# Kernel tuning notes

Hardware: AMD Instinct MI355X
Metric: run time of the kernel (lower is better)

Reference implementation:

```python
import jax, jax.numpy as jnp
import numpy as np
from jax import lax

B, L, N, D, H = 32, 128, 64, 64, 4
DH = D // H


def lstm_seq(x, Wih, Whh, b, h0, c0):
    # x: [T, B, I]; PyTorch gate order i, f, g, o; bias b = b_ih + b_hh fused.
    def step(carry, xt):
        h, c = carry
        g = xt @ Wih.T + h @ Whh.T + b  # [B, 4D]
        i, f, gg, o = jnp.split(g, 4, axis=-1)
        c = jax.nn.sigmoid(f) * c + jax.nn.sigmoid(i) * jnp.tanh(gg)
        h = jax.nn.sigmoid(o) * jnp.tanh(c)
        return (h, c), h
    _, Hs = lax.scan(step, (h0, c0), x)
    return Hs  # [T, B, D]


def encode_one(x, Wih, Whh, b, pw, pb):
    # x: [T, B, 1] single variable series; per-variable LSTM encoder + temporal attn pool
    z0 = jnp.zeros((x.shape[1], Whh.shape[1]), x.dtype)
    Hs = lstm_seq(x, Wih, Whh, b, z0, z0)        # [T, B, D]
    a = jax.nn.softmax(Hs @ pw + pb, axis=0)      # softmax over time -> [T, B]
    return jnp.einsum('tb,tbd->bd', a, Hs)        # [B, D]


def decode_one(cs, Wih, Whh, b, Wh, bh, Wc, bc, ow, ob):
    # cs: [B, D]; all-zero input sequence of length L
    h0 = jnp.tanh(cs @ Wh.T + bh)
    c0 = jnp.tanh(cs @ Wc.T + bc)
    z = jnp.zeros((L, cs.shape[0], 1), cs.dtype)
    Ys = lstm_seq(z, Wih, Whh, b, h0, c0)         # [L, B, D]
    return Ys @ ow + ob                           # [L, B]


def forward(X, enc_Wih, enc_Whh, enc_b, pool_w, pool_b,
            attn_Wqkv, attn_bqkv, attn_Wo, attn_bo,
            dec_Wih, dec_Whh, dec_b, init_h_W, init_h_b, init_c_W, init_c_b,
            out_w, out_b):
    # ---- per-variable encoders (vmapped over N distinct weight sets) ----
    Xe = jnp.transpose(X[:, :L - 1, :], (2, 1, 0))[..., None]  # [N, L-1, B, 1]
    C = jax.vmap(encode_one)(Xe, enc_Wih, enc_Whh, enc_b, pool_w, pool_b)  # [N, B, D]
    C = jnp.transpose(C, (1, 0, 2))  # [B, N, D]

    # ---- cross-variable MHSA (nn.MultiheadAttention, dropout=0) ----
    qkv = C @ attn_Wqkv.T + attn_bqkv            # [B, N, 3D]
    q, k, v = jnp.split(qkv, 3, axis=-1)
    def heads(t):
        return jnp.transpose(t.reshape(B, N, H, DH), (0, 2, 1, 3))  # [B, H, N, DH]
    q, k, v = heads(q), heads(k), heads(v)
    attn = jax.nn.softmax(jnp.einsum('bhnd,bhmd->bhnm', q, k) / np.sqrt(DH), axis=-1)
    o = jnp.einsum('bhnm,bhmd->bhnd', attn, v)
    o = jnp.transpose(o, (0, 2, 1, 3)).reshape(B, N, D)
    C_star = o @ attn_Wo.T + attn_bo             # [B, N, D]

    # ---- per-variable decoders (vmapped over N) ----
    Cs = jnp.transpose(C_star, (1, 0, 2))        # [N, B, D]
    O = jax.vmap(decode_one)(Cs, dec_Wih, dec_Whh, dec_b,
                             init_h_W, init_h_b, init_c_W, init_c_b,
                             out_w, out_b)       # [N, L, B]
    recon = jnp.transpose(O[:, :L - 1, :], (2, 1, 0))  # [B, L-1, N]
    pred = O[:, L - 1, :].T                             # [B, N]
    return recon, pred, C_star


def setup_inputs() -> dict:
    key = jax.random.key(0)
    ks = jax.random.split(key, 20)
    s = 1.0 / np.sqrt(D)
    rn = lambda k, shape: (jax.random.normal(k, shape, jnp.float32) * s)
    return {
        'X': jax.random.normal(ks[0], (B, L, N), jnp.float32),
        'enc_Wih': rn(ks[1], (N, 4 * D, 1)),
        'enc_Whh': rn(ks[2], (N, 4 * D, D)),
        'enc_b': rn(ks[3], (N, 4 * D)),
        'pool_w': rn(ks[4], (N, D)),
        'pool_b': rn(ks[5], (N,)),
        'attn_Wqkv': rn(ks[6], (3 * D, D)),
        'attn_bqkv': rn(ks[7], (3 * D,)),
        'attn_Wo': rn(ks[8], (D, D)),
        'attn_bo': rn(ks[9], (D,)),
        'dec_Wih': rn(ks[10], (N, 4 * D, 1)),
        'dec_Whh': rn(ks[11], (N, 4 * D, D)),
        'dec_b': rn(ks[12], (N, 4 * D)),
        'init_h_W': rn(ks[13], (N, D, D)),
        'init_h_b': rn(ks[14], (N, D)),
        'init_c_W': rn(ks[15], (N, D, D)),
        'init_c_b': rn(ks[16], (N, D)),
        'out_w': rn(ks[17], (N, D)),
        'out_b': rn(ks[18], (N,)),
    }


def reference(X, enc_Wih, enc_Whh, enc_b, pool_w, pool_b,
              attn_Wqkv, attn_bqkv, attn_Wo, attn_bo,
              dec_Wih, dec_Whh, dec_b, init_h_W, init_h_b, init_c_W, init_c_b,
              out_w, out_b):
    return forward(X, enc_Wih, enc_Whh, enc_b, pool_w, pool_b,
                   attn_Wqkv, attn_bqkv, attn_Wo, attn_bo,
                   dec_Wih, dec_Whh, dec_b, init_h_W, init_h_b, init_c_W, init_c_b,
                   out_w, out_b)
```

## Files before the change

### kernel.cpp

```cpp
#include <hip/hip_runtime.h>
#include <cstddef>

#define BB   32
#define LL   128
#define NN   64
#define DD   64
#define HH   4
#define DHH  16
#define G4   256
#define BPG  4

__device__ __forceinline__ float sigmoidf_(float x) {
    return 1.0f / (1.0f + __expf(-x));
}
__device__ __forceinline__ float tanhf_(float x) {
    float e = __expf(2.0f * x);
    return 1.0f - 2.0f / (e + 1.0f);
}

__global__ __launch_bounds__(256, 2)
void enc_kernel(const float* __restrict__ X,
                const float* __restrict__ Wih,
                const float* __restrict__ Whh,
                const float* __restrict__ bias,
                const float* __restrict__ poolw,
                const float* __restrict__ poolb,
                float* __restrict__ Cws)
{
    const int n  = blockIdx.x >> 3;
    const int bg = blockIdx.x & 7;
    const int b0 = bg * BPG;
    const int tid = threadIdx.x;
    const int j0 = tid & 63;
    const int bq = tid >> 6;

    __shared__ __align__(16) float hl[64 * BPG];
    __shared__ float gl[G4 * 5];
    __shared__ float xs[BPG][LL];

    float4 w4[16];
    const float4* wrow =
        reinterpret_cast<const float4*>(Whh + ((size_t)n * G4 + tid) * DD);
#pragma unroll
    for (int i = 0; i < 16; ++i) w4[i] = wrow[i];

    const float wih = Wih[n * G4 + tid];
    const float bj  = bias[n * G4 + tid];
    const float pwj = poolw[n * DD + j0];
    const float pbn = poolb[n];

    for (int i = tid; i < BPG * LL; i += 256) {
        int bb = i >> 7, t = i & 127;
        xs[bb][t] = (t < LL - 1)
            ? X[(size_t)(b0 + bb) * (LL * NN) + (size_t)t * NN + n] : 0.0f;
    }
    hl[tid] = 0.0f;
    float c = 0.0f;
    float m = -1e30f, s = 0.0f, pa = 0.0f;
    __syncthreads();

    for (int t = 0; t < LL - 1; ++t) {
        float a0 = fmaf(xs[0][t], wih, bj);
        float a1 = fmaf(xs[1][t], wih, bj);
        float a2 = fmaf(xs[2][t], wih, bj);
        float a3 = fmaf(xs[3][t], wih, bj);
#pragma unroll
        for (int k4 = 0; k4 < 16; ++k4) {
#pragma unroll
            for (int q = 0; q < 4; ++q) {
                const float4 h4 =
                    *reinterpret_cast<const float4*>(&hl[(k4 * 4 + q) * 4]);
                const float wk = (q == 0) ? w4[k4].x : (q == 1) ? w4[k4].y
                               : (q == 2) ? w4[k4].z : w4[k4].w;
                a0 = fmaf(wk, h4.x, a0);
                a1 = fmaf(wk, h4.y, a1);
                a2 = fmaf(wk, h4.z, a2);
                a3 = fmaf(wk, h4.w, a3);
            }
        }
        {
            float* g = &gl[tid * 5];
            g[0] = a0; g[1] = a1; g[2] = a2; g[3] = a3;
        }
        __syncthreads();

        const float gi = gl[(j0      ) * 5 + bq];
        const float gf = gl[(j0 +  64) * 5 + bq];
        const float gg = gl[(j0 + 128) * 5 + bq];
        const float go = gl[(j0 + 192) * 5 + bq];
        c = sigmoidf_(gf) * c + sigmoidf_(gi) * tanhf_(gg);
        const float h = sigmoidf_(go) * tanhf_(c);

        float p = h * pwj;
#pragma unroll
        for (int off = 32; off >= 1; off >>= 1) p += __shfl_xor(p, off, 64);
        const float score = p + pbn;

        const float mn   = fmaxf(m, score);
        const float corr = __expf(m - mn);
        const float wgt  = __expf(score - mn);
        s  = s * corr + wgt;
        pa = pa * corr + wgt * h;
        m  = mn;

        hl[j0 * 4 + bq] = h;
        __syncthreads();
    }

    Cws[(size_t)(b0 + bq) * (NN * DD) + (size_t)n * DD + j0] = pa / s;
}

__global__ __launch_bounds__(256)
void attn_kernel(const float* __restrict__ Cws,
                 const float* __restrict__ Wqkv,
                 const float* __restrict__ bqkv,
                 float* __restrict__ Ows)
{
    const int b = blockIdx.x >> 2;
    const int h = blockIdx.x & 3;
    const int tid = threadIdx.x;

    __shared__ float Cl[64][65];
    __shared__ float Wl[48][65];
    __shared__ float biasl[48];
    __shared__ float ql[64][17], kl[64][17], vl[64][17];
    __shared__ float sl[64][65];

    for (int i = tid; i < 64 * 64; i += 256)
        Cl[i >> 6][i & 63] = Cws[(size_t)b * (NN * DD) + i];
    for (int i = tid; i < 48 * 64; i += 256) {
        int row = i >> 6, col = i & 63;
        int grp = row >> 4, r = row & 15;
        Wl[row][col] = Wqkv[(size_t)(grp * 64 + h * 16 + r) * DD + col];
    }
    if (tid < 48) {
        int grp = tid >> 4, r = tid & 15;
        biasl[tid] = bqkv[grp * 64 + h * 16 + r];
    }
    __syncthreads();

    for (int i = tid; i < 3 * 64 * 16; i += 256) {
        int sec = i >> 10;
        int rem = i & 1023;
        int nn = rem >> 4, dh = rem & 15;
        float acc = biasl[sec * 16 + dh];
        const float* wr = &Wl[sec * 16 + dh][0];
#pragma unroll 16
        for (int k = 0; k < 64; ++k) acc = fmaf(Cl[nn][k], wr[k], acc);
        if      (sec == 0) ql[nn][dh] = acc;
        else if (sec == 1) kl[nn][dh] = acc;
        else               vl[nn][dh] = acc;
    }
    __syncthreads();

    for (int i = tid; i < 64 * 64; i += 256) {
        int nn = i >> 6, mm = i & 63;
        float acc = 0.0f;
#pragma unroll
        for (int d = 0; d < 16; ++d) acc = fmaf(ql[nn][d], kl[mm][d], acc);
        sl[nn][mm] = acc * 0.25f;
    }
    __syncthreads();

    if (tid < 64) {
        float mx = -1e30f;
        for (int mm = 0; mm < 64; ++mm) mx = fmaxf(mx, sl[tid][mm]);
        float ss = 0.0f;
        for (int mm = 0; mm < 64; ++mm) {
            float e = __expf(sl[tid][mm] - mx);
            sl[tid][mm] = e;
            ss += e;
        }
        float inv = 1.0f / ss;
        for (int mm = 0; mm < 64; ++mm) sl[tid][mm] *= inv;
    }
    __syncthreads();

    for (int i = tid; i < 64 * 16; i += 256) {
        int nn = i >> 4, dh = i & 15;
        float acc = 0.0f;
#pragma unroll 16
        for (int mm = 0; mm < 64; ++mm) acc = fmaf(sl[nn][mm], vl[mm][dh], acc);
        Ows[(size_t)b * (NN * DD) + (size_t)nn * DD + h * 16 + dh] = acc;
    }
}

__global__ __launch_bounds__(256)
void proj_kernel(const float* __restrict__ Ows,
                 const float* __restrict__ Wo,
                 const float* __restrict__ bo,
                 float* __restrict__ Cstar)
{
    const int b = blockIdx.x;
    const int tid = threadIdx.x;
    __shared__ float Ol[64][65];
    __shared__ float Wl[64][65];

    for (int i = tid; i < 64 * 64; i += 256) {
        Ol[i >> 6][i & 63] = Ows[(size_t)b * (NN * DD) + i];
        Wl[i >> 6][i & 63] = Wo[i];
    }
    __syncthreads();

    for (int i = tid; i < 64 * 64; i += 256) {
        int nn = i >> 6, d = i & 63;
        float acc = bo[d];
#pragma unroll 16
        for (int k = 0; k < 64; ++k) acc = fmaf(Ol[nn][k], Wl[d][k], acc);
        Cstar[(size_t)b * (NN * DD) + i] = acc;
    }
}

__global__ __launch_bounds__(256, 2)
void dec_kernel(const float* __restrict__ Whh,
                const float* __restrict__ bias,
                const float* __restrict__ WhI,
                const float* __restrict__ bhI,
                const float* __restrict__ WcI,
                const float* __restrict__ bcI,
                const float* __restrict__ ow,
                const float* __restrict__ ob,
                const float* __restrict__ Cstar,
                float* __restrict__ recon,
                float* __restrict__ pred)
{
    const int n  = blockIdx.x >> 3;
    const int bg = blockIdx.x & 7;
    const int b0 = bg * BPG;
    const int tid = threadIdx.x;
    const int j0 = tid & 63;
    const int bq = tid >> 6;

    __shared__ __align__(16) float hl[64 * BPG];
    __shared__ float gl[G4 * 5];
    __shared__ float csl[BPG][64];

    float4 w4[16];
    const float4* wrow =
        reinterpret_cast<const float4*>(Whh + ((size_t)n * G4 + tid) * DD);
#pragma unroll
    for (int i = 0; i < 16; ++i) w4[i] = wrow[i];
    const float bj  = bias[n * G4 + tid];
    const float owj = ow[n * DD + j0];
    const float obn = ob[n];

    {
        int bb = tid >> 6, d = tid & 63;
        csl[bb][d] = Cstar[(size_t)(b0 + bb) * (NN * DD) + (size_t)n * DD + d];
    }
    __syncthreads();

    float ah = bhI[n * DD + j0];
    float ac = bcI[n * DD + j0];
    {
        const float4* whr =
            reinterpret_cast<const float4*>(WhI + ((size_t)n * DD + j0) * DD);
        const float4* wcr =
            reinterpret_cast<const float4*>(WcI + ((size_t)n * DD + j0) * DD);
#pragma unroll
        for (int i = 0; i < 16; ++i) {
            float4 wh = whr[i], wc = wcr[i];
            ah = fmaf(wh.x, csl[bq][i * 4 + 0], ah);
            ah = fmaf(wh.y, csl[bq][i * 4 + 1], ah);
            ah = fmaf(wh.z, csl[bq][i * 4 + 2], ah);
            ah = fmaf(wh.w, csl[bq][i * 4 + 3], ah);
            ac = fmaf(wc.x, csl[bq][i * 4 + 0], ac);
            ac = fmaf(wc.y, csl[bq][i * 4 + 1], ac);
            ac = fmaf(wc.z, csl[bq][i * 4 + 2], ac);
            ac = fmaf(wc.w, csl[bq][i * 4 + 3], ac);
        }
    }
    float c = tanhf_(ac);
    hl[j0 * 4 + bq] = tanhf_(ah);
    __syncthreads();

    for (int t = 0; t < LL; ++t) {
        float a0 = bj, a1 = bj, a2 = bj, a3 = bj;
#pragma unroll
        for (int k4 = 0; k4 < 16; ++k4) {
#pragma unroll
            for (int q = 0; q < 4; ++q) {
                const float4 h4 =
                    *reinterpret_cast<const float4*>(&hl[(k4 * 4 + q) * 4]);
                const float wk = (q == 0) ? w4[k4].x : (q == 1) ? w4[k4].y
                               : (q == 2) ? w4[k4].z : w4[k4].w;
                a0 = fmaf(wk, h4.x, a0);
                a1 = fmaf(wk, h4.y, a1);
                a2 = fmaf(wk, h4.z, a2);
                a3 = fmaf(wk, h4.w, a3);
            }
        }
        {
            float* g = &gl[tid * 5];
            g[0] = a0; g[1] = a1; g[2] = a2; g[3] = a3;
        }
        __syncthreads();

        const float gi = gl[(j0      ) * 5 + bq];
        const float gf = gl[(j0 +  64) * 5 + bq];
        const float gg = gl[(j0 + 128) * 5 + bq];
        const float go = gl[(j0 + 192) * 5 + bq];
        c = sigmoidf_(gf) * c + sigmoidf_(gi) * tanhf_(gg);
        const float h = sigmoidf_(go) * tanhf_(c);

        float p = h * owj;
#pragma unroll
        for (int off = 32; off >= 1; off >>= 1) p += __shfl_xor(p, off, 64);
        if (j0 == 0) {
            const float y = p + obn;
            const int b = b0 + bq;
            if (t < LL - 1)
                recon[(size_t)b * ((LL - 1) * NN) + (size_t)t * NN + n] = y;
            else
                pred[(size_t)b * NN + n] = y;
        }

        hl[j0 * 4 + bq] = h;
        __syncthreads();
    }
}

extern "C" void kernel_launch(void* const* d_in, const int* in_sizes, int n_in,
                              void* d_out, int out_size, void* d_ws, size_t ws_size,
                              hipStream_t stream) {
    (void)in_sizes; (void)n_in; (void)out_size; (void)ws_size;

    const float* X         = (const float*)d_in[0];
    const float* enc_Wih   = (const float*)d_in[1];
    const float* enc_Whh   = (const float*)d_in[2];
    const float* enc_b     = (const float*)d_in[3];
    const float* pool_w    = (const float*)d_in[4];
    const float* pool_b    = (const float*)d_in[5];
    const float* attn_Wqkv = (const float*)d_in[6];
    const float* attn_bqkv = (const float*)d_in[7];
    const float* attn_Wo   = (const float*)d_in[8];
    const float* attn_bo   = (const float*)d_in[9];
    const float* dec_Whh   = (const float*)d_in[11];
    const float* dec_b     = (const float*)d_in[12];
    const float* init_h_W  = (const float*)d_in[13];
    const float* init_h_b  = (const float*)d_in[14];
    const float* init_c_W  = (const float*)d_in[15];
    const float* init_c_b  = (const float*)d_in[16];
    const float* out_w     = (const float*)d_in[17];
    const float* out_b     = (const float*)d_in[18];

    float* out   = (float*)d_out;
    float* recon = out;
    float* pred  = out + (size_t)BB * (LL - 1) * NN;
    float* cstar = pred + (size_t)BB * NN;

    float* Cws = (float*)d_ws;
    float* Ows = Cws + (size_t)BB * NN * DD;

    enc_kernel<<<dim3(NN * 8), dim3(256), 0, stream>>>(
        X, enc_Wih, enc_Whh, enc_b, pool_w, pool_b, Cws);

    attn_kernel<<<dim3(BB * HH), dim3(256), 0, stream>>>(
        Cws, attn_Wqkv, attn_bqkv, Ows);

    proj_kernel<<<dim3(BB), dim3(256), 0, stream>>>(
        Ows, attn_Wo, attn_bo, cstar);

    dec_kernel<<<dim3(NN * 8), dim3(256), 0, stream>>>(
        dec_Whh, dec_b, init_h_W, init_h_b, init_c_W, init_c_b,
        out_w, out_b, cstar, recon, pred);
}
```

Before: 481.1 us.

## Run each LSTM as a single wave per (variable,batch) with readlane broadcasts

Restructures the encoder and decoder LSTM kernels so each 64-thread block handles one (variable, batch) pair. Each lane owns one hidden unit and keeps all four gate rows of Whh in registers as packed float2 pairs. The hidden state is broadcast with readlane instead of going through shared memory, which removes both __syncthreads per timestep and the LDS gate exchange. The cost is that weights are loaded 32 times more often, register pressure is very high (256 floats per lane for weights), and the decoder init is split into its own kernel. Packed v2f FMAs are used to issue two gate FMAs per instruction.

```diff
diff --git a/kernel.cpp b/kernel.cpp
--- a/kernel.cpp
+++ b/kernel.cpp
@@ -6,10 +6,12 @@
 #define NN   64
 #define DD   64
 #define HH   4
-#define DHH  16
-#define G4   256
-#define BPG  4
-
+
+typedef float v2f __attribute__((ext_vector_type(2)));
+
+__device__ __forceinline__ float bcast(float v, int l) {
+    return __int_as_float(__builtin_amdgcn_readlane(__float_as_int(v), l));
+}
 __device__ __forceinline__ float sigmoidf_(float x) {
     return 1.0f / (1.0f + __expf(-x));
 }
@@ -18,7 +20,29 @@
     return 1.0f - 2.0f / (e + 1.0f);
 }
 
-__global__ __launch_bounds__(256, 2)
+__device__ __forceinline__ void load_gate_rows(const float* __restrict__ W,
+                                               int n, int u,
+                                               v2f (&wif)[64], v2f (&wgo)[64]) {
+    const float4* Ri = reinterpret_cast<const float4*>(W + ((size_t)n * 256 + u      ) * 64);
+    const float4* Rf = reinterpret_cast<const float4*>(W + ((size_t)n * 256 + u +  64) * 64);
+    const float4* Rg = reinterpret_cast<const float4*>(W + ((size_t)n * 256 + u + 128) * 64);
+    const float4* Ro = reinterpret_cast<const float4*>(W + ((size_t)n * 256 + u + 192) * 64);
+#pragma unroll
+    for (int q = 0; q < 16; ++q) {
+        float4 a = Ri[q], b = Rf[q];
+        wif[4 * q + 0] = v2f{a.x, b.x};
+        wif[4 * q + 1] = v2f{a.y, b.y};
+        wif[4 * q + 2] = v2f{a.z, b.z};
+        wif[4 * q + 3] = v2f{a.w, b.w};
+        float4 c = Rg[q], d = Ro[q];
+        wgo[4 * q + 0] = v2f{c.x, d.x};
+        wgo[4 * q + 1] = v2f{c.y, d.y};
+        wgo[4 * q + 2] = v2f{c.z, d.z};
+        wgo[4 * q + 3] = v2f{c.w, d.w};
+    }
+}
+
+__global__ __launch_bounds__(64)
 void enc_kernel(const float* __restrict__ X,
                 const float* __restrict__ Wih,
                 const float* __restrict__ Whh,
@@ -27,71 +51,46 @@
                 const float* __restrict__ poolb,
                 float* __restrict__ Cws)
 {
-    const int n  = blockIdx.x >> 3;
-    const int bg = blockIdx.x & 7;
-    const int b0 = bg * BPG;
-    const int tid = threadIdx.x;
-    const int j0 = tid & 63;
-    const int bq = tid >> 6;
-
-    __shared__ __align__(16) float hl[64 * BPG];
-    __shared__ float gl[G4 * 5];
-    __shared__ float xs[BPG][LL];
-
-    float4 w4[16];
-    const float4* wrow =
-        reinterpret_cast<const float4*>(Whh + ((size_t)n * G4 + tid) * DD);
-#pragma unroll
-    for (int i = 0; i < 16; ++i) w4[i] = wrow[i];
-
-    const float wih = Wih[n * G4 + tid];
-    const float bj  = bias[n * G4 + tid];
-    const float pwj = poolw[n * DD + j0];
+    const int n = blockIdx.x >> 5;
+    const int b = blockIdx.x & 31;
+    const int u = threadIdx.x;
+
+    v2f wif[64], wgo[64];
+    load_gate_rows(Whh, n, u, wif, wgo);
+
+    const float* Bn = bias + n * 256;
+    const v2f bif = {Bn[u],       Bn[u +  64]};
+    const v2f bgo = {Bn[u + 128], Bn[u + 192]};
+    const float* Wn = Wih + n * 256;
+    const v2f xif = {Wn[u],       Wn[u +  64]};
+    const v2f xgo = {Wn[u + 128], Wn[u + 192]};
+    const float pwu = poolw[n * DD + u];
     const float pbn = poolb[n];
 
-    for (int i = tid; i < BPG * LL; i += 256) {
-        int bb = i >> 7, t = i & 127;
-        xs[bb][t] = (t < LL - 1)
-            ? X[(size_t)(b0 + bb) * (LL * NN) + (size_t)t * NN + n] : 0.0f;
-    }
-    hl[tid] = 0.0f;
-    float c = 0.0f;
+    const float x0 = X[(size_t)b * (LL * NN) + (size_t)u * NN + n];
+    const float x1 = X[(size_t)b * (LL * NN) + (size_t)(u + 64) * NN + n];
+
+    float h = 0.0f, c = 0.0f;
     float m = -1e30f, s = 0.0f, pa = 0.0f;
-    __syncthreads();
-
+
+#pragma unroll 1
     for (int t = 0; t < LL - 1; ++t) {
-        float a0 = fmaf(xs[0][t], wih, bj);
-        float a1 = fmaf(xs[1][t], wih, bj);
-        float a2 = fmaf(xs[2][t], wih, bj);
-        float a3 = fmaf(xs[3][t], wih, bj);
-#pragma unroll
-        for (int k4 = 0; k4 < 16; ++k4) {
-#pragma unroll
-            for (int q = 0; q < 4; ++q) {
-                const float4 h4 =
-                    *reinterpret_cast<const float4*>(&hl[(k4 * 4 + q) * 4]);
-                const float wk = (q == 0) ? w4[k4].x : (q == 1) ? w4[k4].y
-                               : (q == 2) ? w4[k4].z : w4[k4].w;
-                a0 = fmaf(wk, h4.x, a0);
-                a1 = fmaf(wk, h4.y, a1);
-                a2 = fmaf(wk, h4.z, a2);
-                a3 = fmaf(wk, h4.w, a3);
-            }
+        const float xt = bcast((t < 64) ? x0 : x1, t & 63);
+        v2f aif = __builtin_elementwise_fma(xif, v2f{xt, xt}, bif);
+        v2f ago = __builtin_elementwise_fma(xgo, v2f{xt, xt}, bgo);
+#pragma unroll
+        for (int k = 0; k < 64; ++k) {
+            const float hk = bcast(h, k);
+            const v2f hh = {hk, hk};
+            aif = __builtin_elementwise_fma(wif[k], hh, aif);
+            ago = __builtin_elementwise_fma(wgo[k], hh, ago);
         }
-        {
-            float* g = &gl[tid * 5];
-            g[0] = a0; g[1] = a1; g[2] = a2; g[3] = a3;
-        }
-        __syncthreads();
-
-        const float gi = gl[(j0      ) * 5 + bq];
-        const float gf = gl[(j0 +  64) * 5 + bq];
-        const float gg = gl[(j0 + 128) * 5 + bq];
-        const float go = gl[(j0 + 192) * 5 + bq];
-        c = sigmoidf_(gf) * c + sigmoidf_(gi) * tanhf_(gg);
-        const float h = sigmoidf_(go) * tanhf_(c);
-
-        float p = h * pwj;
+        const float gi = sigmoidf_(aif.x), gf = sigmoidf_(aif.y);
+        const float gg = tanhf_(ago.x),   go = sigmoidf_(ago.y);
+        c = gf * c + gi * gg;
+        h = go * tanhf_(c);
+
+        float p = h * pwu;
 #pragma unroll
         for (int off = 32; off >= 1; off >>= 1) p += __shfl_xor(p, off, 64);
         const float score = p + pbn;
@@ -102,12 +101,9 @@
         s  = s * corr + wgt;
         pa = pa * corr + wgt * h;
         m  = mn;
-
-        hl[j0 * 4 + bq] = h;
-        __syncthreads();
-    }
-
-    Cws[(size_t)(b0 + bq) * (NN * DD) + (size_t)n * DD + j0] = pa / s;
+    }
+
+    Cws[(size_t)b * (NN * DD) + (size_t)n * DD + u] = pa / s;
 }
 
 __global__ __launch_bounds__(256)
@@ -211,112 +207,93 @@
     }
 }
 
-__global__ __launch_bounds__(256, 2)
+__global__ __launch_bounds__(64)
+void dec_init_kernel(const float* __restrict__ Cstar,
+                     const float* __restrict__ WhI,
+                     const float* __restrict__ bhI,
+                     const float* __restrict__ WcI,
+                     const float* __restrict__ bcI,
+                     float* __restrict__ H0,
+                     float* __restrict__ C0)
+{
+    const int n = blockIdx.x >> 5;
+    const int b = blockIdx.x & 31;
+    const int u = threadIdx.x;
+
+    const float cs = Cstar[(size_t)b * (NN * DD) + (size_t)n * DD + u];
+    const float4* Rh = reinterpret_cast<const float4*>(WhI + ((size_t)n * DD + u) * DD);
+    const float4* Rc = reinterpret_cast<const float4*>(WcI + ((size_t)n * DD + u) * DD);
+    float ah = bhI[n * DD + u];
+    float ac = bcI[n * DD + u];
+#pragma unroll
+    for (int q = 0; q < 16; ++q) {
+        const float4 wh = Rh[q], wc = Rc[q];
+        float k0 = bcast(cs, 4 * q + 0);
+        float k1 = bcast(cs, 4 * q + 1);
+        float k2 = bcast(cs, 4 * q + 2);
+        float k3 = bcast(cs, 4 * q + 3);
+        ah = fmaf(wh.x, k0, ah); ah = fmaf(wh.y, k1, ah);
+        ah = fmaf(wh.z, k2, ah); ah = fmaf(wh.w, k3, ah);
+        ac = fmaf(wc.x, k0, ac); ac = fmaf(wc.y, k1, ac);
+        ac = fmaf(wc.z, k2, ac); ac = fmaf(wc.w, k3, ac);
+    }
+    const size_t idx = ((size_t)n * BB + b) * DD + u;
+    H0[idx] = tanhf_(ah);
+    C0[idx] = tanhf_(ac);
+}
+
+__global__ __launch_bounds__(64)
 void dec_kernel(const float* __restrict__ Whh,
                 const float* __restrict__ bias,
-                const float* __restrict__ WhI,
-                const float* __restrict__ bhI,
-                const float* __restrict__ WcI,
-                const float* __restrict__ bcI,
                 const float* __restrict__ ow,
                 const float* __restrict__ ob,
-                const float* __restrict__ Cstar,
+                const float* __restrict__ H0,
+                const float* __restrict__ C0,
                 float* __restrict__ recon,
                 float* __restrict__ pred)
 {
-    const int n  = blockIdx.x >> 3;
-    const int bg = blockIdx.x & 7;
-    const int b0 = bg * BPG;
-    const int tid = threadIdx.x;
-    const int j0 = tid & 63;
-    const int bq = tid >> 6;
-
-    __shared__ __align__(16) float hl[64 * BPG];
-    __shared__ float gl[G4 * 5];
-    __shared__ float csl[BPG][64];
-
-    float4 w4[16];
-    const float4* wrow =
-        reinterpret_cast<const float4*>(Whh + ((size_t)n * G4 + tid) * DD);
-#pragma unroll
-    for (int i = 0; i < 16; ++i) w4[i] = wrow[i];
-    const float bj  = bias[n * G4 + tid];
-    const float owj = ow[n * DD + j0];
+    const int n = blockIdx.x >> 5;
+    const int b = blockIdx.x & 31;
+    const int u = threadIdx.x;
+
+    v2f wif[64], wgo[64];
+    load_gate_rows(Whh, n, u, wif, wgo);
+
+    const float* Bn = bias + n * 256;
+    const v2f bif = {Bn[u],       Bn[u +  64]};
+    const v2f bgo = {Bn[u + 128], Bn[u + 192]};
+    const float owu = ow[n * DD + u];
     const float obn = ob[n];
 
-    {
-        int bb = tid >> 6, d = tid & 63;
-        csl[bb][d] = Cstar[(size_t)(b0 + bb) * (NN * DD) + (size_t)n * DD + d];
-    }
-    __syncthreads();
-
-    float ah = bhI[n * DD + j0];
-    float ac = bcI[n * DD + j0];
-    {
-        const float4* whr =
-            reinterpret_cast<const float4*>(WhI + ((size_t)n * DD + j0) * DD);
-        const float4* wcr =
-            reinterpret_cast<const float4*>(WcI + ((size_t)n * DD + j0) * DD);
-#pragma unroll
-        for (int i = 0; i < 16; ++i) {
-            float4 wh = whr[i], wc = wcr[i];
-            ah = fmaf(wh.x, csl[bq][i * 4 + 0], ah);
-            ah = fmaf(wh.y, csl[bq][i * 4 + 1], ah);
-            ah = fmaf(wh.z, csl[bq][i * 4 + 2], ah);
-            ah = fmaf(wh.w, csl[bq][i * 4 + 3], ah);
-            ac = fmaf(wc.x, csl[bq][i * 4 + 0], ac);
-            ac = fmaf(wc.y, csl[bq][i * 4 + 1], ac);
-            ac = fmaf(wc.z, csl[bq][i * 4 + 2], ac);
-            ac = fmaf(wc.w, csl[bq][i * 4 + 3], ac);
+    const size_t idx = ((size_t)n * BB + b) * DD + u;
+    float h = H0[idx];
+    float c = C0[idx];
+
+#pragma unroll 1
+    for (int t = 0; t < LL; ++t) {
+        v2f aif = bif, ago = bgo;
+#pragma unroll
+        for (int k = 0; k < 64; ++k) {
+            const float hk = bcast(h, k);
+            const v2f hh = {hk, hk};
+            aif = __builtin_elementwise_fma(wif[k], hh, aif);
+            ago = __builtin_elementwise_fma(wgo[k], hh, ago);
         }
-    }
-    float c = tanhf_(ac);
-    hl[j0 * 4 + bq] = tanhf_(ah);
-    __syncthreads();
-
-    for (int t = 0; t < LL; ++t) {
-        float a0 = bj, a1 = bj, a2 = bj, a3 = bj;
-#pragma unroll
-        for (int k4 = 0; k4 < 16; ++k4) {
-#pragma unroll
-            for (int q = 0; q < 4; ++q) {
-                const float4 h4 =
-                    *reinterpret_cast<const float4*>(&hl[(k4 * 4 + q) * 4]);
-                const float wk = (q == 0) ? w4[k4].x : (q == 1) ? w4[k4].y
-                               : (q == 2) ? w4[k4].z : w4[k4].w;
-                a0 = fmaf(wk, h4.x, a0);
-                a1 = fmaf(wk, h4.y, a1);
-                a2 = fmaf(wk, h4.z, a2);
-                a3 = fmaf(wk, h4.w, a3);
-            }
-        }
-        {
-            float* g = &gl[tid * 5];
-            g[0] = a0; g[1] = a1; g[2] = a2; g[3] = a3;
-        }
-        __syncthreads();
-
-        const float gi = gl[(j0      ) * 5 + bq];
-        const float gf = gl[(j0 +  64) * 5 + bq];
-        const float gg = gl[(j0 + 128) * 5 + bq];
-        const float go = gl[(j0 + 192) * 5 + bq];
-        c = sigmoidf_(gf) * c + sigmoidf_(gi) * tanhf_(gg);
-        const float h = sigmoidf_(go) * tanhf_(c);
-
-        float p = h * owj;
+        const float gi = sigmoidf_(aif.x), gf = sigmoidf_(aif.y);
+        const float gg = tanhf_(ago.x),   go = sigmoidf_(ago.y);
+        c = gf * c + gi * gg;
+        h = go * tanhf_(c);
+
+        float p = h * owu;
 #pragma unroll
         for (int off = 32; off >= 1; off >>= 1) p += __shfl_xor(p, off, 64);
-        if (j0 == 0) {
+        if (u == 0) {
             const float y = p + obn;
-            const int b = b0 + bq;
             if (t < LL - 1)
                 recon[(size_t)b * ((LL - 1) * NN) + (size_t)t * NN + n] = y;
             else
                 pred[(size_t)b * NN + n] = y;
         }
-
-        hl[j0 * 4 + bq] = h;
-        __syncthreads();
     }
 }
 
@@ -351,8 +328,10 @@
 
     float* Cws = (float*)d_ws;
     float* Ows = Cws + (size_t)BB * NN * DD;
-
-    enc_kernel<<<dim3(NN * 8), dim3(256), 0, stream>>>(
+    float* H0 = Cws;
+    float* C0 = Ows;
+
+    enc_kernel<<<dim3(NN * BB), dim3(64), 0, stream>>>(
         X, enc_Wih, enc_Whh, enc_b, pool_w, pool_b, Cws);
 
     attn_kernel<<<dim3(BB * HH), dim3(256), 0, stream>>>(
@@ -361,7 +340,9 @@
     proj_kernel<<<dim3(BB), dim3(256), 0, stream>>>(
         Ows, attn_Wo, attn_bo, cstar);
 
-    dec_kernel<<<dim3(NN * 8), dim3(256), 0, stream>>>(
-        dec_Whh, dec_b, init_h_W, init_h_b, init_c_W, init_c_b,
-        out_w, out_b, cstar, recon, pred);
-}
+    dec_init_kernel<<<dim3(NN * BB), dim3(64), 0, stream>>>(
+        cstar, init_h_W, init_h_b, init_c_W, init_c_b, H0, C0);
+
+    dec_kernel<<<dim3(NN * BB), dim3(64), 0, stream>>>(
+        dec_Whh, dec_b, out_w, out_b, H0, C0, recon, pred);
+}
```

After: 580.5 us. 20.7% more time.
